# Kernel tuning notes

Hardware: AMD Instinct MI355X
Metric: run time of the kernel (lower is better)

The kernel has to match this reference:

```python
import jax, jax.numpy as jnp
import numpy as np

H = 32          # query heads
KVH = 8         # kv heads (GQA)
D = 128         # head dim
GROUP = 128     # quantization group size along K
THETA = 10000.0 # RoPE base


def dequant_fp4(codes, scales):
    """FP4 E2M1-style dequant: w = (code - 8) * 0.5 * per-group scale.
    codes: [K, N] int32 in [0,16); scales: [K//GROUP, N] float32."""
    K, N = codes.shape
    g = K // GROUP
    w = (codes.astype(jnp.float32) - 8.0) * 0.5
    return (w.reshape(g, GROUP, N) * scales[:, None, :]).reshape(K, N)


def apply_rope(x, pos):
    """x: [B, S, h, D]; rotate-half RoPE."""
    half = D // 2
    inv_freq = 1.0 / (THETA ** (jnp.arange(half, dtype=jnp.float32) / half))
    ang = pos.astype(jnp.float32)[:, None] * inv_freq[None, :]  # [S, half]
    cos = jnp.cos(ang)[None, :, None, :]
    sin = jnp.sin(ang)[None, :, None, :]
    x1, x2 = x[..., :half], x[..., half:]
    return jnp.concatenate([x1 * cos - x2 * sin, x2 * cos + x1 * sin], axis=-1)


def setup_inputs() -> dict:
    key = jax.random.key(0)
    ks = jax.random.split(key, 9)
    B, S, HID = 1, 2048, H * D
    KV = KVH * D
    x = jax.random.normal(ks[0], (B, S, HID), dtype=jnp.float32)
    q_codes = jax.random.randint(ks[1], (HID, HID), 0, 16, dtype=jnp.int32)
    k_codes = jax.random.randint(ks[2], (HID, KV), 0, 16, dtype=jnp.int32)
    v_codes = jax.random.randint(ks[3], (HID, KV), 0, 16, dtype=jnp.int32)
    o_codes = jax.random.randint(ks[4], (HID, HID), 0, 16, dtype=jnp.int32)
    g = HID // GROUP
    mk = lambda k, n: jax.random.uniform(k, (g, n), dtype=jnp.float32) * 0.02 + 1e-3
    q_scales = mk(ks[5], HID)
    k_scales = mk(ks[6], KV)
    v_scales = mk(ks[7], KV)
    o_scales = mk(ks[8], HID)
    return {"x": x, "q_codes": q_codes, "k_codes": k_codes, "v_codes": v_codes,
            "o_codes": o_codes, "q_scales": q_scales, "k_scales": k_scales,
            "v_scales": v_scales, "o_scales": o_scales}


def reference(x, q_codes, k_codes, v_codes, o_codes,
              q_scales, k_scales, v_scales, o_scales):
    B, S, _ = x.shape
    Wq = dequant_fp4(q_codes, q_scales)  # [HID, HID]
    Wk = dequant_fp4(k_codes, k_scales)  # [HID, KVH*D]
    Wv = dequant_fp4(v_codes, v_scales)
    Wo = dequant_fp4(o_codes, o_scales)

    q = (x @ Wq).reshape(B, S, H, D)
    k = (x @ Wk).reshape(B, S, KVH, D)
    v = (x @ Wv).reshape(B, S, KVH, D)

    pos = jnp.arange(S)
    q = apply_rope(q, pos)
    k = apply_rope(k, pos)

    # GQA: expand kv heads to query heads (this is what reading the shared
    # KV cache per query-head group computes)
    rep = H // KVH
    k = jnp.repeat(k, rep, axis=2)  # [B, S, H, D]
    v = jnp.repeat(v, rep, axis=2)

    scale = 1.0 / jnp.sqrt(jnp.float32(D))
    scores = jnp.einsum('bqhd,bkhd->bhqk', q, k) * scale  # [B, H, S, S]
    causal = jnp.tril(jnp.ones((S, S), dtype=bool))
    scores = jnp.where(causal[None, None], scores, jnp.float32(-1e30))
    probs = jax.nn.softmax(scores, axis=-1)
    attn = jnp.einsum('bhqk,bkhd->bqhd', probs, v).reshape(B, S, H * D)
    return attn @ Wo
```

## Files before the change

kernel.cpp:

```cpp
#include <hip/hip_runtime.h>

typedef unsigned short u16;
typedef __attribute__((ext_vector_type(4))) float f32x4;
typedef __attribute__((ext_vector_type(16))) float f32x16;
typedef __attribute__((ext_vector_type(4))) unsigned short u16x4;
typedef __attribute__((ext_vector_type(4))) unsigned u32x4;
typedef __attribute__((ext_vector_type(2))) unsigned u32x2;
typedef __attribute__((ext_vector_type(8))) short bf16x8;

#define S_LEN 2048
#define NH 32
#define NKVH 8
#define DHEAD 128
#define HID 4096
#define KVW 1024
#define QKVW 6144

__device__ __forceinline__ u16 f2bf(float f) {
  unsigned u = __float_as_uint(f);
  u = u + 0x7fffu + ((u >> 16) & 1u);
  return (u16)(u >> 16);
}
__device__ __forceinline__ float bf2f(u16 h) {
  return __uint_as_float(((unsigned)h) << 16);
}
__device__ __forceinline__ void async16(void* lds, const void* g) {
  __builtin_amdgcn_global_load_lds((const __attribute__((address_space(1))) void*)g,
                                   (__attribute__((address_space(3))) void*)lds, 16, 0, 0);
}
__device__ __forceinline__ f32x4 mfma16(bf16x8 a, bf16x8 b, f32x4 c) {
  return __builtin_amdgcn_mfma_f32_16x16x32_bf16(a, b, c, 0, 0, 0);
}
__device__ __forceinline__ f32x16 mfma32(bf16x8 a, bf16x8 b, f32x16 c) {
  return __builtin_amdgcn_mfma_f32_32x32x16_bf16(a, b, c, 0, 0, 0);
}
__device__ __forceinline__ unsigned cvtpk(float a, float b) {
  unsigned r;
  asm("v_cvt_pk_bf16_f32 %0, %1, %2" : "=v"(r) : "v"(a), "v"(b));
  return r;
}
__device__ __forceinline__ u32x2 pl32(unsigned a, unsigned b) {
  return __builtin_amdgcn_permlane32_swap(a, b, 0, 0);
}

__global__ __launch_bounds__(256) void f2bf4_kernel(const float* __restrict__ in,
                                                    u16* __restrict__ out) {
  size_t i = ((size_t)blockIdx.x * 256 + threadIdx.x) * 4;
  f32x4 v = *(const f32x4*)(in + i);
  u16x4 o;
  o.x = f2bf(v.x); o.y = f2bf(v.y); o.z = f2bf(v.z); o.w = f2bf(v.w);
  *(u16x4*)(out + i) = o;
}

__global__ __launch_bounds__(256) void dequant_t_kernel(const int* __restrict__ codes,
                                                        const float* __restrict__ scales,
                                                        u16* __restrict__ Wt,
                                                        int K, int N) {
  __shared__ float tile[32][33];
  const int tx = threadIdx.x & 31, ty = threadIdx.x >> 5;
  const int k0 = blockIdx.x * 32, n0 = blockIdx.y * 32;
  const float sc = scales[(size_t)(k0 >> 7) * N + n0 + tx];
#pragma unroll
  for (int i = 0; i < 4; ++i) {
    int k = k0 + ty + i * 8;
    int c = codes[(size_t)k * N + n0 + tx];
    tile[ty + i * 8][tx] = ((float)c - 8.0f) * 0.5f * sc;
  }
  __syncthreads();
#pragma unroll
  for (int i = 0; i < 4; ++i) {
    int n = n0 + ty + i * 8;
    Wt[(size_t)n * K + k0 + tx] = f2bf(tile[tx][ty + i * 8]);
  }
}

template <int NI, int OUTF32>
__global__ __launch_bounds__(512, 2) void gemm_w(const u16* __restrict__ A, int lda,
                                                 const u16* __restrict__ Bt, int ldb,
                                                 void* __restrict__ Cv, int ldc, int K) {
  constexpr int BN = NI * 32;
  constexpr int NB = NI / 2;
  constexpr int BSLOT = BN * 128;
  extern __shared__ char lds[];
  char* Bbase = lds + 65536;
  const int tid = threadIdx.x, w = tid >> 6, lane = tid & 63;
  const int lo = lane & 15, hi = lane >> 4;
  const int wm = w >> 1, wn = w & 1;
  const int id = blockIdx.x;
  const int g = id & 7, r = id >> 3;
  const int bm = r >> 2, bn = g * 4 + (r & 3);
  const int m0 = bm * 256, n0 = bn * BN;

  const int srow = tid >> 3, schunk = (tid & 7) ^ (srow & 7);
  const char* Ab = (const char*)(A + (size_t)(m0 + srow) * lda) + schunk * 16;
  const char* Bb = (const char*)(Bt + (size_t)(n0 + srow) * ldb) + schunk * 16;

  f32x4 acc[4][NI];
#pragma unroll
  for (int i = 0; i < 4; ++i)
#pragma unroll
    for (int j = 0; j < NI; ++j) acc[i][j] = (f32x4){0.f, 0.f, 0.f, 0.f};

  auto stageA = [&](int buf, int k1) {
#pragma unroll
    for (int u = 0; u < 2; ++u) {
      char* dst = lds + buf * 32768 + u * 8192 + w * 1024;
      async16(dst, Ab + ((size_t)(u * 64) * lda + k1) * 2);
      async16(dst + 16384, Ab + ((size_t)(u * 64 + 128) * lda + k1) * 2);
    }
  };
  auto stageB = [&](int slot, int k1) {
#pragma unroll
    for (int j = 0; j < NB; ++j)
      async16(Bbase + slot * BSLOT + j * 8192 + w * 1024,
              Bb + ((size_t)(j * 64) * ldb + k1) * 2);
  };

  const int xm = (lo & 7) << 4;
  const int aro = (wm >> 1) * 16384 + (wm & 1) * 8192 + lo * 128;
  int bofs[NI];
#pragma unroll
  for (int ni = 0; ni < NI; ++ni) {
    int n = wn * (NI * 16) + ni * 16 + lo;
    bofs[ni] = (n >> 6) * 8192 + (n & 63) * 128;
  }

  auto ldfrags = [&](const char* As, const char* Bs, int kk, bf16x8* Afo, bf16x8* Bfo) {
    const int ck = (kk * 64 + hi * 16) ^ xm;
#pragma unroll
    for (int i = 0; i < 4; ++i) Afo[i] = *(const bf16x8*)(As + aro + i * 2048 + ck);
#pragma unroll
    for (int ni = 0; ni < NI; ++ni) Bfo[ni] = *(const bf16x8*)(Bs + bofs[ni] + ck);
  };

  stageA(0, 0);
  stageB(0, 0);
  stageB(1, 64);
  asm volatile("s_waitcnt vmcnt(%0)" ::"i"(NB) : "memory");
  __builtin_amdgcn_s_barrier();

  bf16x8 Afc[4], Bfc[NI], Afn[4], Bfn[NI];
  ldfrags(lds, Bbase, 0, Afc, Bfc);

  const int KT = K >> 6;
  int ab = 0, bb = 0;
  for (int t = 0; t < KT; ++t) {
    const char* As = lds + ab * 32768;
    const char* Bs = Bbase + bb * BSLOT;
    const bool m1 = t + 1 < KT, m2 = t + 2 < KT;
    int bs2 = bb + 2; if (bs2 >= 3) bs2 -= 3;
    int bn1 = bb + 1; if (bn1 >= 3) bn1 -= 3;
    if (m1) stageA(ab ^ 1, (t + 1) << 6);
    ldfrags(As, Bs, 1, Afn, Bfn);
    __builtin_amdgcn_sched_barrier(0);
    __builtin_amdgcn_s_setprio(1);
#pragma unroll
    for (int i = 0; i < 4; ++i)
#pragma unroll
      for (int ni = 0; ni < NI; ++ni)
        acc[i][ni] = mfma16(Afc[i], Bfc[ni], acc[i][ni]);
    __builtin_amdgcn_s_setprio(0);
    if (m2) stageB(bs2, (t + 2) << 6);
    __builtin_amdgcn_s_setprio(1);
#pragma unroll
    for (int i = 0; i < 4; ++i)
#pragma unroll
      for (int ni = 0; ni < NI; ++ni)
        acc[i][ni] = mfma16(Afn[i], Bfn[ni], acc[i][ni]);
    __builtin_amdgcn_s_setprio(0);
    if (m1) {
      if (m2) asm volatile("s_waitcnt vmcnt(%0)" ::"i"(NB) : "memory");
      else    asm volatile("s_waitcnt vmcnt(0)" ::: "memory");
      __builtin_amdgcn_s_barrier();
      ldfrags(lds + (ab ^ 1) * 32768, Bbase + bn1 * BSLOT, 0, Afc, Bfc);
      __builtin_amdgcn_sched_barrier(0);
    }
    ab ^= 1;
    if (++bb == 3) bb = 0;
  }
#pragma unroll
  for (int mi = 0; mi < 4; ++mi)
#pragma unroll
    for (int ni = 0; ni < NI; ++ni) {
      size_t row = (size_t)(m0 + wm * 64 + mi * 16 + hi * 4);
      size_t col = (size_t)(n0 + wn * (NI * 16) + ni * 16 + lo);
#pragma unroll
      for (int rr = 0; rr < 4; ++rr) {
        size_t idx = (row + rr) * ldc + col;
        if (OUTF32) ((float*)Cv)[idx] = acc[mi][ni][rr];
        else ((u16*)Cv)[idx] = f2bf(acc[mi][ni][rr]);
      }
    }
}

__global__ void rope_tab_kernel(float* __restrict__ ctab, float* __restrict__ stab) {
  int s = blockIdx.x, d = threadIdx.x;
  float inv = exp2f(-(float)d * 0.2076205059304601f);
  float ang = (float)s * inv;
  ctab[s * 64 + d] = cosf(ang);
  stab[s * 64 + d] = sinf(ang);
}

__global__ __launch_bounds__(256) void rope_kernel(u16* __restrict__ qkv,
                                                   const float* __restrict__ ctab,
                                                   const float* __restrict__ stab) {
  int s = blockIdx.x;
  int head = blockIdx.y * 4 + (threadIdx.x >> 6);
  int d = threadIdx.x & 63;
  int col = head < NH ? head * DHEAD + d : HID + (head - NH) * DHEAD + d;
  size_t base = (size_t)s * QKVW + col;
  float c = ctab[s * 64 + d], sn = stab[s * 64 + d];
  float x1 = bf2f(qkv[base]);
  float x2 = bf2f(qkv[base + 64]);
  qkv[base] = f2bf(x1 * c - x2 * sn);
  qkv[base + 64] = f2bf(x2 * c + x1 * sn);
}

__global__ __launch_bounds__(256) void vtrans_kernel(const u16* __restrict__ qkv,
                                                     u16* __restrict__ Vt) {
  __shared__ u16 tile[32][33];
  const int tx = threadIdx.x & 31, ty = threadIdx.x >> 5;
  const int s0 = blockIdx.x * 32, c0 = blockIdx.y * 32;
#pragma unroll
  for (int i = 0; i < 4; ++i)
    tile[ty + i * 8][tx] = qkv[(size_t)(s0 + ty + i * 8) * QKVW + (HID + KVW) + c0 + tx];
  __syncthreads();
#pragma unroll
  for (int i = 0; i < 4; ++i)
    Vt[(size_t)(c0 + ty + i * 8) * S_LEN + s0 + tx] = tile[tx][ty + i * 8];
}

__global__ __launch_bounds__(256, 2) void attn_kernel(const u16* __restrict__ qkv,
                                                      const u16* __restrict__ Vt,
                                                      u16* __restrict__ attnO) {
  __shared__ alignas(16) u16 Ks[2][64 * 128];
  __shared__ alignas(16) u16 Vs[2][128 * 64];
  const int tid = threadIdx.x, w = tid >> 6, lane = tid & 63;
  const int l31 = lane & 31, hi5 = lane >> 5;
  const int bx = blockIdx.x, hd = blockIdx.y, kvh = hd >> 2;
  const int qb = (hd < 16) ? (15 - bx) : bx;
  const int qrow0 = qb * 128 + w * 32;
  const int qg = qrow0 + l31;
  const u16* Kbase = qkv + HID + kvh * DHEAD;
  const u16* Vbase = Vt + (size_t)kvh * DHEAD * S_LEN;
  const int krow = w * 4 + (lane >> 4), kscn = lane & 15;
  const int vrow = w * 8 + (lane >> 3), vscn = lane & 7;

  auto stage = [&](int buf, int kt) {
#pragma unroll
    for (int i = 0; i < 4; ++i) {
      int kr = i * 16 + krow;
      async16((char*)&Ks[buf][0] + (i * 16 + w * 4) * 256,
              (const char*)(Kbase + (size_t)(kt * 64 + kr) * QKVW + (kscn ^ (kr & 7)) * 8));
      int vr = i * 32 + vrow;
      async16((char*)&Vs[buf][0] + (i * 32 + w * 8) * 128,
              (const char*)(Vbase + (size_t)vr * S_LEN + kt * 64 + (vscn ^ (vr & 7)) * 8));
    }
  };

  bf16x8 qf[8];
  {
    const u16* qp = qkv + (size_t)qg * QKVW + hd * DHEAD + hi5 * 8;
    const float qs = 0.08838834764831845f * 1.4426950408889634f;
#pragma unroll
    for (int dsl = 0; dsl < 8; ++dsl) {
      bf16x8 v = *(const bf16x8*)(qp + dsl * 16);
#pragma unroll
      for (int j = 0; j < 8; ++j) v[j] = (short)f2bf(bf2f((u16)v[j]) * qs);
      qf[dsl] = v;
    }
  }
  f32x16 oacc[4];
#pragma unroll
  for (int db = 0; db < 4; ++db)
#pragma unroll
    for (int r = 0; r < 16; ++r) oacc[db][r] = 0.f;
  float m_run = -1e30f, l_run = 0.f;

  const int nt = 2 * (qb + 1);
  stage(0, 0);
  __syncthreads();
  for (int kt = 0; kt < nt; ++kt) {
    const int cur = kt & 1;
    if (kt + 1 < nt) stage(cur ^ 1, kt + 1);
    if (kt * 64 <= qrow0 + 31) {
      const char* Kc = (const char*)&Ks[cur][0];
      const char* Vc = (const char*)&Vs[cur][0];
      bf16x8 kf0[8], kf1[8];
#pragma unroll
      for (int dsl = 0; dsl < 8; ++dsl) {
        kf0[dsl] = *(const bf16x8*)(Kc + l31 * 256 + ((2 * dsl + hi5) ^ (l31 & 7)) * 16);
        kf1[dsl] = *(const bf16x8*)(Kc + (32 + l31) * 256 +
                                    ((2 * dsl + hi5) ^ ((32 + l31) & 7)) * 16);
      }
      f32x16 st[2];
#pragma unroll
      for (int r = 0; r < 16; ++r) { st[0][r] = 0.f; st[1][r] = 0.f; }
      __builtin_amdgcn_s_setprio(1);
#pragma unroll
      for (int dsl = 0; dsl < 8; ++dsl) {
        st[0] = mfma32(kf0[dsl], qf[dsl], st[0]);
        st[1] = mfma32(kf1[dsl], qf[dsl], st[1]);
      }
      __builtin_amdgcn_s_setprio(0);
      if (kt >= 2 * qb) {
#pragma unroll
        for (int blk = 0; blk < 2; ++blk)
#pragma unroll
          for (int r = 0; r < 16; ++r) {
            int kpg = kt * 64 + blk * 32 + (r & 3) + 8 * (r >> 2) + 4 * hi5;
            st[blk][r] = (kpg <= qg) ? st[blk][r] : -1e30f;
          }
      }
      float tm[16];
#pragma unroll
      for (int r = 0; r < 16; ++r) tm[r] = fmaxf(st[0][r], st[1][r]);
#pragma unroll
      for (int off = 8; off >= 1; off >>= 1)
#pragma unroll
        for (int r = 0; r < off; ++r) tm[r] = fmaxf(tm[r], tm[r + off]);
      float mloc;
      {
        u32x2 rr = pl32(__float_as_uint(tm[0]), __float_as_uint(tm[0]));
        mloc = fmaxf(__uint_as_float(rr.x), __uint_as_float(rr.y));
      }
      if (!__all(mloc - m_run <= 8.0f)) {
        float mn = fmaxf(m_run, mloc);
        float alpha = exp2f(m_run - mn);
        m_run = mn;
        l_run *= alpha;
#pragma unroll
        for (int db = 0; db < 4; ++db)
#pragma unroll
          for (int r = 0; r < 16; ++r) oacc[db][r] *= alpha;
      }
#pragma unroll
      for (int blk = 0; blk < 2; ++blk)
#pragma unroll
        for (int r = 0; r < 16; ++r) st[blk][r] = exp2f(st[blk][r] - m_run);
      float ts[16];
#pragma unroll
      for (int r = 0; r < 16; ++r) ts[r] = st[0][r] + st[1][r];
#pragma unroll
      for (int off = 8; off >= 1; off >>= 1)
#pragma unroll
        for (int r = 0; r < off; ++r) ts[r] += ts[r + off];
      {
        u32x2 rr = pl32(__float_as_uint(ts[0]), __float_as_uint(ts[0]));
        l_run += __uint_as_float(rr.x) + __uint_as_float(rr.y);
      }
      bf16x8 pf[4];
#pragma unroll
      for (int s = 0; s < 4; ++s) {
        const int blk = s >> 1, r0 = (s & 1) * 8;
        unsigned a0 = cvtpk(st[blk][r0 + 0], st[blk][r0 + 1]);
        unsigned a1 = cvtpk(st[blk][r0 + 2], st[blk][r0 + 3]);
        unsigned b0 = cvtpk(st[blk][r0 + 4], st[blk][r0 + 5]);
        unsigned b1 = cvtpk(st[blk][r0 + 6], st[blk][r0 + 7]);
        u32x2 r0p = pl32(a0, b0);
        u32x2 r1p = pl32(a1, b1);
        u32x4 t; t.x = r0p.x; t.y = r1p.x; t.z = r0p.y; t.w = r1p.y;
        pf[s] = __builtin_bit_cast(bf16x8, t);
      }
      __builtin_amdgcn_s_setprio(1);
#pragma unroll
      for (int s = 0; s < 4; ++s) {
        bf16x8 vf[4];
#pragma unroll
        for (int db = 0; db < 4; ++db) {
          const int row = db * 32 + l31;
          vf[db] = *(const bf16x8*)(Vc + row * 128 + ((2 * s + hi5) ^ (row & 7)) * 16);
        }
#pragma unroll
        for (int db = 0; db < 4; ++db) oacc[db] = mfma32(vf[db], pf[s], oacc[db]);
      }
      __builtin_amdgcn_s_setprio(0);
    }
    __syncthreads();
  }
  float linv = 1.0f / l_run;
  u16* op = attnO + (size_t)qg * HID + hd * DHEAD;
#pragma unroll
  for (int db = 0; db < 4; ++db)
#pragma unroll
    for (int g = 0; g < 4; ++g) {
      u16x4 o4;
#pragma unroll
      for (int r2 = 0; r2 < 4; ++r2) o4[r2] = f2bf(oacc[db][g * 4 + r2] * linv);
      *(u16x4*)(op + db * 32 + 8 * g + 4 * hi5) = o4;
    }
}

extern "C" void kernel_launch(void* const* d_in, const int* in_sizes, int n_in,
                              void* d_out, int out_size, void* d_ws, size_t ws_size,
                              hipStream_t stream) {
  const float* x = (const float*)d_in[0];
  const int* qc = (const int*)d_in[1];
  const int* kc = (const int*)d_in[2];
  const int* vc = (const int*)d_in[3];
  const int* oc = (const int*)d_in[4];
  const float* qs = (const float*)d_in[5];
  const float* ks = (const float*)d_in[6];
  const float* vs = (const float*)d_in[7];
  const float* os = (const float*)d_in[8];
  float* out = (float*)d_out;
  char* ws = (char*)d_ws;

  u16* xb    = (u16*)(ws);
  u16* qkv   = (u16*)(ws + 16777216);
  u16* attnb = (u16*)(ws + 41943040);
  u16* Vt    = (u16*)(ws + 58720256);
  u16* Wbig  = (u16*)(ws + 62914560);
  float* ctab = (float*)Vt;
  float* stab = (float*)(ws + 58720256 + 524288);

  f2bf4_kernel<<<8192, 256, 0, stream>>>(x, xb);
  dequant_t_kernel<<<dim3(128, 128), 256, 0, stream>>>(qc, qs, Wbig, HID, HID);
  dequant_t_kernel<<<dim3(128, 32), 256, 0, stream>>>(kc, ks, Wbig + (size_t)HID * HID, HID, KVW);
  dequant_t_kernel<<<dim3(128, 32), 256, 0, stream>>>(vc, vs, Wbig + (size_t)(HID + KVW) * HID, HID, KVW);
  rope_tab_kernel<<<2048, 64, 0, stream>>>(ctab, stab);
  gemm_w<6, 0><<<256, 512, 139264, stream>>>(xb, HID, Wbig, HID, qkv, QKVW, HID);
  rope_kernel<<<dim3(S_LEN, (NH + NKVH) / 4), 256, 0, stream>>>(qkv, ctab, stab);
  vtrans_kernel<<<dim3(64, 32), 256, 0, stream>>>(qkv, Vt);
  attn_kernel<<<dim3(16, 32), 256, 0, stream>>>(qkv, Vt, attnb);
  dequant_t_kernel<<<dim3(128, 128), 256, 0, stream>>>(oc, os, Wbig, HID, HID);
  gemm_w<4, 1><<<256, 512, 114688, stream>>>(attnb, HID, Wbig, HID, out, HID, HID);
}
```

Measured before the change: 323.5 us.

## Restructure GEMM main loop into four barrier-synchronized sub-phases with interleaved loads

Replaces the double-buffered register fragment scheme (current/next fragments prefetched across iterations) with four sub-phases per K tile. Each sub-phase loads two A fragments and, when needed, the B fragments, issues the global async stages at fixed points, then waits on lgkmcnt and runs MFMAs. Two workgroup barriers per sub-phase keep the waves in lockstep. This lowers register pressure and may align waves in a ping-pong style, but it adds many barriers and removes the overlap of LDS reads with MFMA work.

```diff
diff --git a/kernel.cpp b/kernel.cpp
--- a/kernel.cpp
+++ b/kernel.cpp
@@ -125,22 +125,11 @@
     bofs[ni] = (n >> 6) * 8192 + (n & 63) * 128;
   }
 
-  auto ldfrags = [&](const char* As, const char* Bs, int kk, bf16x8* Afo, bf16x8* Bfo) {
-    const int ck = (kk * 64 + hi * 16) ^ xm;
-#pragma unroll
-    for (int i = 0; i < 4; ++i) Afo[i] = *(const bf16x8*)(As + aro + i * 2048 + ck);
-#pragma unroll
-    for (int ni = 0; ni < NI; ++ni) Bfo[ni] = *(const bf16x8*)(Bs + bofs[ni] + ck);
-  };
-
   stageA(0, 0);
   stageB(0, 0);
   stageB(1, 64);
   asm volatile("s_waitcnt vmcnt(%0)" ::"i"(NB) : "memory");
   __builtin_amdgcn_s_barrier();
-
-  bf16x8 Afc[4], Bfc[NI], Afn[4], Bfn[NI];
-  ldfrags(lds, Bbase, 0, Afc, Bfc);
 
   const int KT = K >> 6;
   int ab = 0, bb = 0;
@@ -149,31 +138,34 @@
     const char* Bs = Bbase + bb * BSLOT;
     const bool m1 = t + 1 < KT, m2 = t + 2 < KT;
     int bs2 = bb + 2; if (bs2 >= 3) bs2 -= 3;
-    int bn1 = bb + 1; if (bn1 >= 3) bn1 -= 3;
-    if (m1) stageA(ab ^ 1, (t + 1) << 6);
-    ldfrags(As, Bs, 1, Afn, Bfn);
-    __builtin_amdgcn_sched_barrier(0);
-    __builtin_amdgcn_s_setprio(1);
-#pragma unroll
-    for (int i = 0; i < 4; ++i)
-#pragma unroll
-      for (int ni = 0; ni < NI; ++ni)
-        acc[i][ni] = mfma16(Afc[i], Bfc[ni], acc[i][ni]);
-    __builtin_amdgcn_s_setprio(0);
-    if (m2) stageB(bs2, (t + 2) << 6);
-    __builtin_amdgcn_s_setprio(1);
-#pragma unroll
-    for (int i = 0; i < 4; ++i)
-#pragma unroll
-      for (int ni = 0; ni < NI; ++ni)
-        acc[i][ni] = mfma16(Afn[i], Bfn[ni], acc[i][ni]);
-    __builtin_amdgcn_s_setprio(0);
-    if (m1) {
-      if (m2) asm volatile("s_waitcnt vmcnt(%0)" ::"i"(NB) : "memory");
-      else    asm volatile("s_waitcnt vmcnt(0)" ::: "memory");
+    bf16x8 Bf[NI];
+#pragma unroll
+    for (int q = 0; q < 4; ++q) {
+      const int kk = q >> 1, ih = q & 1;
+      const int ck = (kk * 64 + hi * 16) ^ xm;
+      bf16x8 Af0 = *(const bf16x8*)(As + aro + (ih * 2 + 0) * 2048 + ck);
+      bf16x8 Af1 = *(const bf16x8*)(As + aro + (ih * 2 + 1) * 2048 + ck);
+      if (ih == 0) {
+#pragma unroll
+        for (int ni = 0; ni < NI; ++ni)
+          Bf[ni] = *(const bf16x8*)(Bs + bofs[ni] + ck);
+      }
+      if (q == 0 && m1) stageA(ab ^ 1, (t + 1) << 6);
+      if (q == 2 && m2) stageB(bs2, (t + 2) << 6);
       __builtin_amdgcn_s_barrier();
-      ldfrags(lds + (ab ^ 1) * 32768, Bbase + bn1 * BSLOT, 0, Afc, Bfc);
-      __builtin_amdgcn_sched_barrier(0);
+      asm volatile("s_waitcnt lgkmcnt(0)" ::: "memory");
+      __builtin_amdgcn_s_setprio(1);
+#pragma unroll
+      for (int ni = 0; ni < NI; ++ni) {
+        acc[ih * 2 + 0][ni] = mfma16(Af0, Bf[ni], acc[ih * 2 + 0][ni]);
+        acc[ih * 2 + 1][ni] = mfma16(Af1, Bf[ni], acc[ih * 2 + 1][ni]);
+      }
+      __builtin_amdgcn_s_setprio(0);
+      if (q == 3 && m1) {
+        if (m2) asm volatile("s_waitcnt vmcnt(%0)" ::"i"(NB) : "memory");
+        else    asm volatile("s_waitcnt vmcnt(0)" ::: "memory");
+      }
+      __builtin_amdgcn_s_barrier();
     }
     ab ^= 1;
     if (++bb == 3) bb = 0;
```

Result: slower. 334.4 us (+3.4%).

## Repack K/V into MFMA-fragment layout and drop LDS staging in attention

Applied to the files above, without the earlier changes.

K gets RoPE applied while it is repacked, and V is repacked, into per-kv-head layouts matching the MFMA fragment order. The attention kernel then loads K and V fragments straight from global memory (L2-cached) instead of double-buffering through LDS with block-wide barriers. Each wave runs only its own causal tile count, and blocks are remapped so the heads sharing a kv head are grouped for L2 reuse. The cost is exposed global load latency without async staging, plus an extra repack pass.

```diff
diff --git a/kernel.cpp b/kernel.cpp
--- a/kernel.cpp
+++ b/kernel.cpp
@@ -216,8 +216,27 @@
   qkv[base + 64] = f2bf(x2 * c + x1 * sn);
 }
 
-__global__ __launch_bounds__(256) void vtrans_kernel(const u16* __restrict__ qkv,
-                                                     u16* __restrict__ Vt) {
+__global__ __launch_bounds__(256) void krepack_kernel(const u16* __restrict__ qkv,
+                                                      const float* __restrict__ ctab,
+                                                      const float* __restrict__ stab,
+                                                      u16* __restrict__ Kp) {
+  const int s = blockIdx.x, t = threadIdx.x;
+  const u16* row = qkv + (size_t)s * QKVW + HID;
+#pragma unroll
+  for (int i = 0; i < 4; ++i) {
+    int item = i * 256 + t;
+    int kvh = item >> 7, d = item & 127;
+    int dh = d & 63;
+    float x1 = bf2f(row[kvh * 128 + dh]);
+    float x2 = bf2f(row[kvh * 128 + 64 + dh]);
+    float c = ctab[s * 64 + dh], sn = stab[s * 64 + dh];
+    float val = (d < 64) ? (x1 * c - x2 * sn) : (x2 * c + x1 * sn);
+    Kp[(size_t)kvh * 262144 + (d >> 3) * 16384 + s * 8 + (d & 7)] = f2bf(val);
+  }
+}
+
+__global__ __launch_bounds__(256) void vrepack_kernel(const u16* __restrict__ qkv,
+                                                      u16* __restrict__ Vp) {
   __shared__ u16 tile[32][33];
   const int tx = threadIdx.x & 31, ty = threadIdx.x >> 5;
   const int s0 = blockIdx.x * 32, c0 = blockIdx.y * 32;
@@ -225,38 +244,35 @@
   for (int i = 0; i < 4; ++i)
     tile[ty + i * 8][tx] = qkv[(size_t)(s0 + ty + i * 8) * QKVW + (HID + KVW) + c0 + tx];
   __syncthreads();
-#pragma unroll
-  for (int i = 0; i < 4; ++i)
-    Vt[(size_t)(c0 + ty + i * 8) * S_LEN + s0 + tx] = tile[tx][ty + i * 8];
+  if (threadIdx.x < 128) {
+    const int cl = threadIdx.x & 31, pk = threadIdx.x >> 5;
+    const int dg = c0 + cl;
+    const int kvh = dg >> 7, d = dg & 127;
+    const int pp = (s0 >> 3) + pk;
+    u16 tmp[8];
+#pragma unroll
+    for (int j = 0; j < 8; ++j) tmp[j] = tile[pk * 8 + j][cl];
+    *(bf16x8*)(Vp + (size_t)kvh * 262144 + (size_t)pp * 1024 + d * 8) =
+        *(const bf16x8*)tmp;
+  }
 }
 
 __global__ __launch_bounds__(256, 2) void attn_kernel(const u16* __restrict__ qkv,
-                                                      const u16* __restrict__ Vt,
+                                                      const u16* __restrict__ Kp,
+                                                      const u16* __restrict__ Vp,
                                                       u16* __restrict__ attnO) {
-  __shared__ alignas(16) u16 Ks[2][64 * 128];
-  __shared__ alignas(16) u16 Vs[2][128 * 64];
   const int tid = threadIdx.x, w = tid >> 6, lane = tid & 63;
   const int l31 = lane & 31, hi5 = lane >> 5;
-  const int bx = blockIdx.x, hd = blockIdx.y, kvh = hd >> 2;
-  const int qb = (hd < 16) ? (15 - bx) : bx;
+  const int id = blockIdx.x;
+  const int g = id & 7, r = id >> 3;
+  const int hd = g * 4 + (r & 3);
+  const int qcode = r >> 2;
+  const int qb = (qcode & 1) ? (15 - (qcode >> 1)) : (qcode >> 1);
+  const int kvh = g;
   const int qrow0 = qb * 128 + w * 32;
   const int qg = qrow0 + l31;
-  const u16* Kbase = qkv + HID + kvh * DHEAD;
-  const u16* Vbase = Vt + (size_t)kvh * DHEAD * S_LEN;
-  const int krow = w * 4 + (lane >> 4), kscn = lane & 15;
-  const int vrow = w * 8 + (lane >> 3), vscn = lane & 7;
-
-  auto stage = [&](int buf, int kt) {
-#pragma unroll
-    for (int i = 0; i < 4; ++i) {
-      int kr = i * 16 + krow;
-      async16((char*)&Ks[buf][0] + (i * 16 + w * 4) * 256,
-              (const char*)(Kbase + (size_t)(kt * 64 + kr) * QKVW + (kscn ^ (kr & 7)) * 8));
-      int vr = i * 32 + vrow;
-      async16((char*)&Vs[buf][0] + (i * 32 + w * 8) * 128,
-              (const char*)(Vbase + (size_t)vr * S_LEN + kt * 64 + (vscn ^ (vr & 7)) * 8));
-    }
-  };
+  const u16* Kl = Kp + (size_t)kvh * 262144 + hi5 * 16384 + l31 * 8;
+  const u16* Vl = Vp + (size_t)kvh * 262144 + hi5 * 1024 + l31 * 8;
 
   bf16x8 qf[8];
   {
@@ -274,120 +290,109 @@
 #pragma unroll
   for (int db = 0; db < 4; ++db)
 #pragma unroll
-    for (int r = 0; r < 16; ++r) oacc[db][r] = 0.f;
+    for (int r2 = 0; r2 < 16; ++r2) oacc[db][r2] = 0.f;
   float m_run = -1e30f, l_run = 0.f;
 
-  const int nt = 2 * (qb + 1);
-  stage(0, 0);
-  __syncthreads();
-  for (int kt = 0; kt < nt; ++kt) {
-    const int cur = kt & 1;
-    if (kt + 1 < nt) stage(cur ^ 1, kt + 1);
-    if (kt * 64 <= qrow0 + 31) {
-      const char* Kc = (const char*)&Ks[cur][0];
-      const char* Vc = (const char*)&Vs[cur][0];
-      bf16x8 kf0[8], kf1[8];
-#pragma unroll
-      for (int dsl = 0; dsl < 8; ++dsl) {
-        kf0[dsl] = *(const bf16x8*)(Kc + l31 * 256 + ((2 * dsl + hi5) ^ (l31 & 7)) * 16);
-        kf1[dsl] = *(const bf16x8*)(Kc + (32 + l31) * 256 +
-                                    ((2 * dsl + hi5) ^ ((32 + l31) & 7)) * 16);
-      }
-      f32x16 st[2];
-#pragma unroll
-      for (int r = 0; r < 16; ++r) { st[0][r] = 0.f; st[1][r] = 0.f; }
-      __builtin_amdgcn_s_setprio(1);
-#pragma unroll
-      for (int dsl = 0; dsl < 8; ++dsl) {
-        st[0] = mfma32(kf0[dsl], qf[dsl], st[0]);
-        st[1] = mfma32(kf1[dsl], qf[dsl], st[1]);
-      }
-      __builtin_amdgcn_s_setprio(0);
-      if (kt >= 2 * qb) {
-#pragma unroll
-        for (int blk = 0; blk < 2; ++blk)
-#pragma unroll
-          for (int r = 0; r < 16; ++r) {
-            int kpg = kt * 64 + blk * 32 + (r & 3) + 8 * (r >> 2) + 4 * hi5;
-            st[blk][r] = (kpg <= qg) ? st[blk][r] : -1e30f;
-          }
-      }
-      float tm[16];
-#pragma unroll
-      for (int r = 0; r < 16; ++r) tm[r] = fmaxf(st[0][r], st[1][r]);
-#pragma unroll
-      for (int off = 8; off >= 1; off >>= 1)
-#pragma unroll
-        for (int r = 0; r < off; ++r) tm[r] = fmaxf(tm[r], tm[r + off]);
-      float mloc;
-      {
-        u32x2 rr = pl32(__float_as_uint(tm[0]), __float_as_uint(tm[0]));
-        mloc = fmaxf(__uint_as_float(rr.x), __uint_as_float(rr.y));
-      }
-      if (!__all(mloc - m_run <= 8.0f)) {
-        float mn = fmaxf(m_run, mloc);
-        float alpha = exp2f(m_run - mn);
-        m_run = mn;
-        l_run *= alpha;
-#pragma unroll
-        for (int db = 0; db < 4; ++db)
-#pragma unroll
-          for (int r = 0; r < 16; ++r) oacc[db][r] *= alpha;
-      }
+  const int ntw = (qrow0 >> 6) + 1;
+  for (int kt = 0; kt < ntw; ++kt) {
+    bf16x8 kf0[8], kf1[8];
+#pragma unroll
+    for (int dsl = 0; dsl < 8; ++dsl) {
+      kf0[dsl] = *(const bf16x8*)(Kl + dsl * 32768 + kt * 512);
+      kf1[dsl] = *(const bf16x8*)(Kl + dsl * 32768 + kt * 512 + 256);
+    }
+    f32x16 st[2];
+#pragma unroll
+    for (int r2 = 0; r2 < 16; ++r2) { st[0][r2] = 0.f; st[1][r2] = 0.f; }
+    __builtin_amdgcn_s_setprio(1);
+#pragma unroll
+    for (int dsl = 0; dsl < 8; ++dsl) {
+      st[0] = mfma32(kf0[dsl], qf[dsl], st[0]);
+      st[1] = mfma32(kf1[dsl], qf[dsl], st[1]);
+    }
+    __builtin_amdgcn_s_setprio(0);
+    bf16x8 vf[4][4];
+#pragma unroll
+    for (int s = 0; s < 4; ++s)
+#pragma unroll
+      for (int db = 0; db < 4; ++db)
+        vf[s][db] = *(const bf16x8*)(Vl + kt * 8192 + s * 2048 + db * 256);
+    if (kt >= 2 * qb) {
 #pragma unroll
       for (int blk = 0; blk < 2; ++blk)
 #pragma unroll
-        for (int r = 0; r < 16; ++r) st[blk][r] = exp2f(st[blk][r] - m_run);
-      float ts[16];
-#pragma unroll
-      for (int r = 0; r < 16; ++r) ts[r] = st[0][r] + st[1][r];
-#pragma unroll
-      for (int off = 8; off >= 1; off >>= 1)
-#pragma unroll
-        for (int r = 0; r < off; ++r) ts[r] += ts[r + off];
-      {
-        u32x2 rr = pl32(__float_as_uint(ts[0]), __float_as_uint(ts[0]));
-        l_run += __uint_as_float(rr.x) + __uint_as_float(rr.y);
-      }
-      bf16x8 pf[4];
-#pragma unroll
-      for (int s = 0; s < 4; ++s) {
-        const int blk = s >> 1, r0 = (s & 1) * 8;
-        unsigned a0 = cvtpk(st[blk][r0 + 0], st[blk][r0 + 1]);
-        unsigned a1 = cvtpk(st[blk][r0 + 2], st[blk][r0 + 3]);
-        unsigned b0 = cvtpk(st[blk][r0 + 4], st[blk][r0 + 5]);
-        unsigned b1 = cvtpk(st[blk][r0 + 6], st[blk][r0 + 7]);
-        u32x2 r0p = pl32(a0, b0);
-        u32x2 r1p = pl32(a1, b1);
-        u32x4 t; t.x = r0p.x; t.y = r1p.x; t.z = r0p.y; t.w = r1p.y;
-        pf[s] = __builtin_bit_cast(bf16x8, t);
-      }
-      __builtin_amdgcn_s_setprio(1);
-#pragma unroll
-      for (int s = 0; s < 4; ++s) {
-        bf16x8 vf[4];
-#pragma unroll
-        for (int db = 0; db < 4; ++db) {
-          const int row = db * 32 + l31;
-          vf[db] = *(const bf16x8*)(Vc + row * 128 + ((2 * s + hi5) ^ (row & 7)) * 16);
+        for (int r2 = 0; r2 < 16; ++r2) {
+          int kpg = kt * 64 + blk * 32 + (r2 & 3) + 8 * (r2 >> 2) + 4 * hi5;
+          st[blk][r2] = (kpg <= qg) ? st[blk][r2] : -1e30f;
         }
-#pragma unroll
-        for (int db = 0; db < 4; ++db) oacc[db] = mfma32(vf[db], pf[s], oacc[db]);
-      }
-      __builtin_amdgcn_s_setprio(0);
-    }
-    __syncthreads();
+    }
+    float tm[16];
+#pragma unroll
+    for (int r2 = 0; r2 < 16; ++r2) tm[r2] = fmaxf(st[0][r2], st[1][r2]);
+#pragma unroll
+    for (int off = 8; off >= 1; off >>= 1)
+#pragma unroll
+      for (int r2 = 0; r2 < off; ++r2) tm[r2] = fmaxf(tm[r2], tm[r2 + off]);
+    float mloc;
+    {
+      u32x2 rr = pl32(__float_as_uint(tm[0]), __float_as_uint(tm[0]));
+      mloc = fmaxf(__uint_as_float(rr.x), __uint_as_float(rr.y));
+    }
+    if (!__all(mloc - m_run <= 8.0f)) {
+      float mn = fmaxf(m_run, mloc);
+      float alpha = exp2f(m_run - mn);
+      m_run = mn;
+      l_run *= alpha;
+#pragma unroll
+      for (int db = 0; db < 4; ++db)
+#pragma unroll
+        for (int r2 = 0; r2 < 16; ++r2) oacc[db][r2] *= alpha;
+    }
+#pragma unroll
+    for (int blk = 0; blk < 2; ++blk)
+#pragma unroll
+      for (int r2 = 0; r2 < 16; ++r2) st[blk][r2] = exp2f(st[blk][r2] - m_run);
+    float ts[16];
+#pragma unroll
+    for (int r2 = 0; r2 < 16; ++r2) ts[r2] = st[0][r2] + st[1][r2];
+#pragma unroll
+    for (int off = 8; off >= 1; off >>= 1)
+#pragma unroll
+      for (int r2 = 0; r2 < off; ++r2) ts[r2] += ts[r2 + off];
+    {
+      u32x2 rr = pl32(__float_as_uint(ts[0]), __float_as_uint(ts[0]));
+      l_run += __uint_as_float(rr.x) + __uint_as_float(rr.y);
+    }
+    bf16x8 pf[4];
+#pragma unroll
+    for (int s = 0; s < 4; ++s) {
+      const int blk = s >> 1, r0 = (s & 1) * 8;
+      unsigned a0 = cvtpk(st[blk][r0 + 0], st[blk][r0 + 1]);
+      unsigned a1 = cvtpk(st[blk][r0 + 2], st[blk][r0 + 3]);
+      unsigned b0 = cvtpk(st[blk][r0 + 4], st[blk][r0 + 5]);
+      unsigned b1 = cvtpk(st[blk][r0 + 6], st[blk][r0 + 7]);
+      u32x2 r0p = pl32(a0, b0);
+      u32x2 r1p = pl32(a1, b1);
+      u32x4 t2; t2.x = r0p.x; t2.y = r1p.x; t2.z = r0p.y; t2.w = r1p.y;
+      pf[s] = __builtin_bit_cast(bf16x8, t2);
+    }
+    __builtin_amdgcn_s_setprio(1);
+#pragma unroll
+    for (int s = 0; s < 4; ++s)
+#pragma unroll
+      for (int db = 0; db < 4; ++db) oacc[db] = mfma32(vf[s][db], pf[s], oacc[db]);
+    __builtin_amdgcn_s_setprio(0);
   }
   float linv = 1.0f / l_run;
   u16* op = attnO + (size_t)qg * HID + hd * DHEAD;
 #pragma unroll
   for (int db = 0; db < 4; ++db)
 #pragma unroll
-    for (int g = 0; g < 4; ++g) {
+    for (int g2 = 0; g2 < 4; ++g2) {
       u16x4 o4;
 #pragma unroll
-      for (int r2 = 0; r2 < 4; ++r2) o4[r2] = f2bf(oacc[db][g * 4 + r2] * linv);
-      *(u16x4*)(op + db * 32 + 8 * g + 4 * hi5) = o4;
+      for (int r2 = 0; r2 < 4; ++r2) o4[r2] = f2bf(oacc[db][g2 * 4 + r2] * linv);
+      *(u16x4*)(op + db * 32 + 8 * g2 + 4 * hi5) = o4;
     }
 }
 
@@ -413,6 +418,8 @@
   u16* Wbig  = (u16*)(ws + 62914560);
   float* ctab = (float*)Vt;
   float* stab = (float*)(ws + 58720256 + 524288);
+  u16* Kp = (u16*)(ws);
+  u16* Vp = (u16*)(ws + 4194304);
 
   f2bf4_kernel<<<8192, 256, 0, stream>>>(x, xb);
   dequant_t_kernel<<<dim3(128, 128), 256, 0, stream>>>(qc, qs, Wbig, HID, HID);
@@ -420,9 +427,10 @@
   dequant_t_kernel<<<dim3(128, 32), 256, 0, stream>>>(vc, vs, Wbig + (size_t)(HID + KVW) * HID, HID, KVW);
   rope_tab_kernel<<<2048, 64, 0, stream>>>(ctab, stab);
   gemm_w<6, 0><<<256, 512, 139264, stream>>>(xb, HID, Wbig, HID, qkv, QKVW, HID);
-  rope_kernel<<<dim3(S_LEN, (NH + NKVH) / 4), 256, 0, stream>>>(qkv, ctab, stab);
-  vtrans_kernel<<<dim3(64, 32), 256, 0, stream>>>(qkv, Vt);
-  attn_kernel<<<dim3(16, 32), 256, 0, stream>>>(qkv, Vt, attnb);
+  rope_kernel<<<dim3(S_LEN, NH / 4), 256, 0, stream>>>(qkv, ctab, stab);
+  krepack_kernel<<<2048, 256, 0, stream>>>(qkv, ctab, stab, Kp);
+  vrepack_kernel<<<dim3(64, 32), 256, 0, stream>>>(qkv, Vp);
+  attn_kernel<<<512, 256, 0, stream>>>(qkv, Kp, Vp, attnb);
   dequant_t_kernel<<<dim3(128, 128), 256, 0, stream>>>(oc, os, Wbig, HID, HID);
   gemm_w<4, 1><<<256, 512, 114688, stream>>>(attnb, HID, Wbig, HID, out, HID, HID);
 }
```

New measurement: 331.9 us. 1.03x slower.
